# Kernel optimization log

Hardware: AMD Instinct MI355X
Metric: run time of the kernel (lower is better)

## Reference

```python
import jax, jax.numpy as jnp
import numpy as np

BANK_FILTERS = 64
DIM = 128
KSIZE = 3
BATCH = 256


def setup_inputs() -> dict:
    key = jax.random.key(0)
    k1, k2 = jax.random.split(key)
    bank_request = jax.random.normal(k1, (BATCH, BANK_FILTERS), dtype=jnp.float32)
    weight = jax.random.normal(k2, (BANK_FILTERS, DIM, DIM, KSIZE, KSIZE), dtype=jnp.float32)
    return {"bank_request": bank_request, "weight": weight}


def reference(bank_request, weight):
    # softmax over filter bank, then weighted sum of filters -> per-sample kernel
    probs = jax.nn.softmax(bank_request, axis=1)          # (B, F)
    Fb, D1, D2, K1, K2 = weight.shape
    # express as a single GEMM over the filter axis instead of broadcast-mul-reduce
    w2d = weight.reshape(Fb, D1 * D2 * K1 * K2)           # (F, D*D*k*k)
    kernel = probs @ w2d                                   # (B, D*D*k*k)
    return kernel.reshape(bank_request.shape[0], D1, D2, K1, K2)
```

## Files before the change

kernel.cpp:

```cpp
#include <hip/hip_runtime.h>
#include <math.h>

#define BATCH 256
#define FB    64
#define NCOL  147456
#define NCOL4 (NCOL / 4)
#define TPB   256
#define BT    16
#define NBG   (BATCH / BT)
#define NXB   (NCOL / (TPB * 4))
#define PTS   (BT + 4)

#define FMA4(A, S, WV) do { \
    (A).x = fmaf((S), (WV).x, (A).x); \
    (A).y = fmaf((S), (WV).y, (A).y); \
    (A).z = fmaf((S), (WV).z, (A).z); \
    (A).w = fmaf((S), (WV).w, (A).w); \
} while (0)

__global__ __launch_bounds__(TPB, 4) void bank_gemm_fused(
        const float* __restrict__ W, const float* __restrict__ X,
        float* __restrict__ out) {
    __shared__ float pt[FB * PTS];

    const int tid = threadIdx.x;

    const int wg   = blockIdx.y * gridDim.x + blockIdx.x;
    const int xcd  = wg & 7;
    const int slot = wg >> 3;
    const int bx   = xcd * (NXB / 8) + (slot >> 4);
    const int bg   = slot & 15;

    const float4* Wv = (const float4*)W;
    const int c4 = bx * TPB + tid;

    float4 wr0 = Wv[0 * NCOL4 + c4];
    float4 wr1 = Wv[1 * NCOL4 + c4];
    float4 wr2 = Wv[2 * NCOL4 + c4];
    float4 wr3 = Wv[3 * NCOL4 + c4];

    const int wave = tid >> 6;
    const int lane = tid & 63;
#pragma unroll
    for (int r0 = 0; r0 < BT / 4; ++r0) {
        const int r = r0 * 4 + wave;
        float v = X[(bg * BT + r) * FB + lane];
        float m = v;
#pragma unroll
        for (int o = 32; o > 0; o >>= 1) m = fmaxf(m, __shfl_xor(m, o));
        float e = __expf(v - m);
        float s = e;
#pragma unroll
        for (int o = 32; o > 0; o >>= 1) s += __shfl_xor(s, o);
        pt[lane * PTS + r] = e / s;
    }
    __syncthreads();

    float4 acc[BT];
#pragma unroll
    for (int b = 0; b < BT; ++b) acc[b] = make_float4(0.f, 0.f, 0.f, 0.f);

#define STEP(J, WREG) do { \
        const float4 wcur = (WREG); \
        (WREG) = Wv[(f + 4 + (J)) * NCOL4 + c4]; \
        const float4* p4 = (const float4*)&pt[(f + (J)) * PTS]; \
        _Pragma("unroll") \
        for (int q = 0; q < BT / 4; ++q) { \
            const float4 p = p4[q];    \
            FMA4(acc[4 * q + 0], p.x, wcur); \
            FMA4(acc[4 * q + 1], p.y, wcur); \
            FMA4(acc[4 * q + 2], p.z, wcur); \
            FMA4(acc[4 * q + 3], p.w, wcur); \
        } \
    } while (0)

#define TAIL(J, WREG) do { \
        const float4 wcur = (WREG); \
        const float4* p4 = (const float4*)&pt[(f + (J)) * PTS]; \
        _Pragma("unroll") \
        for (int q = 0; q < BT / 4; ++q) { \
            const float4 p = p4[q]; \
            FMA4(acc[4 * q + 0], p.x, wcur); \
            FMA4(acc[4 * q + 1], p.y, wcur); \
            FMA4(acc[4 * q + 2], p.z, wcur); \
            FMA4(acc[4 * q + 3], p.w, wcur); \
        } \
    } while (0)

    for (int f = 0; f < FB - 4; f += 4) {
        STEP(0, wr0);
        STEP(1, wr1);
        STEP(2, wr2);
        STEP(3, wr3);
    }
    {
        const int f = FB - 4;
        TAIL(0, wr0);
        TAIL(1, wr1);
        TAIL(2, wr2);
        TAIL(3, wr3);
    }
#undef STEP
#undef TAIL

    float4* Ov = (float4*)out;
    const int obase = (bg * BT) * NCOL4 + c4;
#pragma unroll
    for (int b = 0; b < BT; ++b) {
        Ov[obase + b * NCOL4] = acc[b];
    }
}

extern "C" void kernel_launch(void* const* d_in, const int* in_sizes, int n_in,
                              void* d_out, int out_size, void* d_ws, size_t ws_size,
                              hipStream_t stream) {
    const float* bank   = (const float*)d_in[0];
    const float* weight = (const float*)d_in[1];
    float* out   = (float*)d_out;
    (void)d_ws; (void)ws_size;

    dim3 grid(NXB, NBG);
    bank_gemm_fused<<<grid, TPB, 0, stream>>>(weight, bank, out);
}
```

Baseline: 246.0 us.

## Split softmax into separate kernel, double batch tile, use nontemporal output stores

Moves the softmax into its own small kernel that writes transposed probabilities to workspace, so the GEMM kernel reads them through uniform global loads instead of shared memory and needs no block barrier. The batch tile per block doubles from 16 to 32, halving how often the weight matrix is re-read. Output stores become nontemporal to limit cache pollution from the large output. In exchange there is an extra kernel launch, register pressure rises from 32 float4 accumulators (launch bounds lowered to 2 blocks), and the XCD remap is adjusted for the new grid shape.

```diff
diff --git a/kernel.cpp b/kernel.cpp
--- a/kernel.cpp
+++ b/kernel.cpp
@@ -6,10 +6,11 @@
 #define NCOL  147456
 #define NCOL4 (NCOL / 4)
 #define TPB   256
-#define BT    16
+#define BT    32
 #define NBG   (BATCH / BT)
 #define NXB   (NCOL / (TPB * 4))
-#define PTS   (BT + 4)
+
+typedef float f4 __attribute__((ext_vector_type(4)));
 
 #define FMA4(A, S, WV) do { \
     (A).x = fmaf((S), (WV).x, (A).x); \
@@ -18,18 +19,30 @@
     (A).w = fmaf((S), (WV).w, (A).w); \
 } while (0)
 
-__global__ __launch_bounds__(TPB, 4) void bank_gemm_fused(
-        const float* __restrict__ W, const float* __restrict__ X,
+__global__ void softmax_t(const float* __restrict__ x, float* __restrict__ pt) {
+    const int b = blockIdx.x;
+    const int lane = threadIdx.x;
+    float v = x[b * FB + lane];
+    float m = v;
+#pragma unroll
+    for (int o = 32; o > 0; o >>= 1) m = fmaxf(m, __shfl_xor(m, o));
+    float e = __expf(v - m);
+    float s = e;
+#pragma unroll
+    for (int o = 32; o > 0; o >>= 1) s += __shfl_xor(s, o);
+    pt[lane * BATCH + b] = e / s;
+}
+
+__global__ __launch_bounds__(TPB, 2) void bank_gemm(
+        const float* __restrict__ W, const float* __restrict__ Pt,
         float* __restrict__ out) {
-    __shared__ float pt[FB * PTS];
-
     const int tid = threadIdx.x;
 
     const int wg   = blockIdx.y * gridDim.x + blockIdx.x;
     const int xcd  = wg & 7;
     const int slot = wg >> 3;
-    const int bx   = xcd * (NXB / 8) + (slot >> 4);
-    const int bg   = slot & 15;
+    const int bx   = xcd * (NXB / 8) + (slot >> 3);
+    const int bg   = slot & (NBG - 1);
 
     const float4* Wv = (const float4*)W;
     const int c4 = bx * TPB + tid;
@@ -39,23 +52,6 @@
     float4 wr2 = Wv[2 * NCOL4 + c4];
     float4 wr3 = Wv[3 * NCOL4 + c4];
 
-    const int wave = tid >> 6;
-    const int lane = tid & 63;
-#pragma unroll
-    for (int r0 = 0; r0 < BT / 4; ++r0) {
-        const int r = r0 * 4 + wave;
-        float v = X[(bg * BT + r) * FB + lane];
-        float m = v;
-#pragma unroll
-        for (int o = 32; o > 0; o >>= 1) m = fmaxf(m, __shfl_xor(m, o));
-        float e = __expf(v - m);
-        float s = e;
-#pragma unroll
-        for (int o = 32; o > 0; o >>= 1) s += __shfl_xor(s, o);
-        pt[lane * PTS + r] = e / s;
-    }
-    __syncthreads();
-
     float4 acc[BT];
 #pragma unroll
     for (int b = 0; b < BT; ++b) acc[b] = make_float4(0.f, 0.f, 0.f, 0.f);
@@ -63,27 +59,27 @@
 #define STEP(J, WREG) do { \
         const float4 wcur = (WREG); \
         (WREG) = Wv[(f + 4 + (J)) * NCOL4 + c4]; \
-        const float4* p4 = (const float4*)&pt[(f + (J)) * PTS]; \
+        const float* pr = Pt + (f + (J)) * BATCH + bg * BT; \
         _Pragma("unroll") \
         for (int q = 0; q < BT / 4; ++q) { \
-            const float4 p = p4[q];    \
-            FMA4(acc[4 * q + 0], p.x, wcur); \
-            FMA4(acc[4 * q + 1], p.y, wcur); \
-            FMA4(acc[4 * q + 2], p.z, wcur); \
-            FMA4(acc[4 * q + 3], p.w, wcur); \
+            const float4 pq = *(const float4*)(pr + 4 * q);  \
+            FMA4(acc[4 * q + 0], pq.x, wcur); \
+            FMA4(acc[4 * q + 1], pq.y, wcur); \
+            FMA4(acc[4 * q + 2], pq.z, wcur); \
+            FMA4(acc[4 * q + 3], pq.w, wcur); \
         } \
     } while (0)
 
 #define TAIL(J, WREG) do { \
         const float4 wcur = (WREG); \
-        const float4* p4 = (const float4*)&pt[(f + (J)) * PTS]; \
+        const float* pr = Pt + (f + (J)) * BATCH + bg * BT; \
         _Pragma("unroll") \
         for (int q = 0; q < BT / 4; ++q) { \
-            const float4 p = p4[q]; \
-            FMA4(acc[4 * q + 0], p.x, wcur); \
-            FMA4(acc[4 * q + 1], p.y, wcur); \
-            FMA4(acc[4 * q + 2], p.z, wcur); \
-            FMA4(acc[4 * q + 3], p.w, wcur); \
+            const float4 pq = *(const float4*)(pr + 4 * q); \
+            FMA4(acc[4 * q + 0], pq.x, wcur); \
+            FMA4(acc[4 * q + 1], pq.y, wcur); \
+            FMA4(acc[4 * q + 2], pq.z, wcur); \
+            FMA4(acc[4 * q + 3], pq.w, wcur); \
         } \
     } while (0)
 
@@ -103,11 +99,13 @@
 #undef STEP
 #undef TAIL
 
-    float4* Ov = (float4*)out;
+    f4* Ov = (f4*)out;
     const int obase = (bg * BT) * NCOL4 + c4;
 #pragma unroll
     for (int b = 0; b < BT; ++b) {
-        Ov[obase + b * NCOL4] = acc[b];
+        f4 val;
+        val.x = acc[b].x; val.y = acc[b].y; val.z = acc[b].z; val.w = acc[b].w;
+        __builtin_nontemporal_store(val, &Ov[obase + b * NCOL4]);
     }
 }
 
@@ -117,8 +115,10 @@
     const float* bank   = (const float*)d_in[0];
     const float* weight = (const float*)d_in[1];
     float* out   = (float*)d_out;
-    (void)d_ws; (void)ws_size;
+    float* probsT = (float*)d_ws;
+
+    softmax_t<<<BATCH, FB, 0, stream>>>(bank, probsT);
 
     dim3 grid(NXB, NBG);
-    bank_gemm_fused<<<grid, TPB, 0, stream>>>(weight, bank, out);
+    bank_gemm<<<grid, TPB, 0, stream>>>(weight, probsT, out);
 }
```

Result: faster. 224.9 us (-8.6%).
